# Performance work log

Hardware: AMD Instinct MI355X
Metric: run time of the kernel (lower is better)

## Reference

```python
import jax, jax.numpy as jnp
import numpy as np

B, IN, OUT, K = 512, 65536, 16384, 32

def setup_inputs() -> dict:
    key = jax.random.key(0)
    k1, k2, k3 = jax.random.split(key, 3)
    x = jax.random.normal(k1, (B, IN), dtype=jnp.float32)
    indices = jax.random.randint(k2, (OUT, K), 0, IN, dtype=jnp.int32)
    weight = jax.random.normal(k3, (OUT, K), dtype=jnp.float32) * 0.1
    bias = jnp.zeros((OUT,), dtype=jnp.float32)
    return {"x": x, "indices": indices, "weight": weight, "bias": bias}

def reference(x, indices, weight, bias):
    # Gather per-output feature subsets: (B, OUT, K)
    x_sel = x[:, indices]
    # Weighted sum over K connections per output, plus bias: (B, OUT)
    out = jnp.einsum('bok,ok->bo', x_sel, weight) + bias
    return out
```

## Files before the change

kernel.cpp:

```cpp
#include <hip/hip_runtime.h>

#define B_DIM   512
#define IN_DIM  65536
#define OUT_DIM 16384
#define K_DIM   32

static __device__ __forceinline__ unsigned short f2bf(float f) {
    unsigned u = __builtin_bit_cast(unsigned, f);
    unsigned r = (u + 0x7FFFu + ((u >> 16) & 1u)) >> 16;
    return (unsigned short)r;
}
static __device__ __forceinline__ float bf2f(unsigned short s) {
    return __builtin_bit_cast(float, ((unsigned)s) << 16);
}

#define TB 128
#define TC 64
#define TS 65

__global__ __launch_bounds__(256) void transpose_bf16_k(const float* __restrict__ x,
                                                        unsigned short* __restrict__ xT) {
    __shared__ float tile[TB][TS];
    const int c0 = blockIdx.x * TC;
    const int b0 = blockIdx.y * TB;
    const int t  = threadIdx.x;

    const int col4 = (t & 15) * 4;
    const int br   = t >> 4;
    #pragma unroll
    for (int rr = 0; rr < TB; rr += 16) {
        float4 v = *(const float4*)(x + (size_t)(b0 + br + rr) * IN_DIM + c0 + col4);
        tile[br + rr][col4 + 0] = v.x;
        tile[br + rr][col4 + 1] = v.y;
        tile[br + rr][col4 + 2] = v.z;
        tile[br + rr][col4 + 3] = v.w;
    }
    __syncthreads();

    const int b4 = (t & 31) * 4;
    const int cw = t >> 5;
    #pragma unroll
    for (int cc = 0; cc < TC; cc += 8) {
        const int c = cc + cw;
        ushort4 p;
        p.x = f2bf(tile[b4 + 0][c]);
        p.y = f2bf(tile[b4 + 1][c]);
        p.z = f2bf(tile[b4 + 2][c]);
        p.w = f2bf(tile[b4 + 3][c]);
        *(ushort4*)(xT + (size_t)(c0 + c) * B_DIM + b0 + b4) = p;
    }
}

#define O_TILE 8
#define SE 520

__global__ __launch_bounds__(128) void sparse_main(const unsigned short* __restrict__ xT,
                                                   const int*   __restrict__ idxp,
                                                   const float* __restrict__ wp,
                                                   const float* __restrict__ biasp,
                                                   float*       __restrict__ out) {
    __shared__ float lds[O_TILE][SE];
    const int o_base = blockIdx.x * O_TILE;
    const int t  = threadIdx.x;
    const int b4 = t * 4;

    float4 acc[O_TILE];
    #pragma unroll
    for (int o = 0; o < O_TILE; ++o) acc[o] = make_float4(0.f, 0.f, 0.f, 0.f);

    for (int k = 0; k < K_DIM; ++k) {
        #pragma unroll
        for (int o = 0; o < O_TILE; ++o) {
            const int   idx = idxp[(o_base + o) * K_DIM + k];
            const float w   = wp [(o_base + o) * K_DIM + k];
            const ushort4 v = *(const ushort4*)(xT + (size_t)idx * B_DIM + b4);
            acc[o].x = fmaf(w, bf2f(v.x), acc[o].x);
            acc[o].y = fmaf(w, bf2f(v.y), acc[o].y);
            acc[o].z = fmaf(w, bf2f(v.z), acc[o].z);
            acc[o].w = fmaf(w, bf2f(v.w), acc[o].w);
        }
    }

    #pragma unroll
    for (int o = 0; o < O_TILE; ++o) {
        const float bv = biasp[o_base + o];
        acc[o].x += bv; acc[o].y += bv; acc[o].z += bv; acc[o].w += bv;
        *(float4*)(&lds[o][b4]) = acc[o];
    }
    __syncthreads();

    #pragma unroll
    for (int p = 0; p < 8; ++p) {
        const int q = p * 512 + t * 4;
        const int b = q >> 3;
        const int o = q & 7;
        float4 v;
        v.x = lds[o + 0][b];
        v.y = lds[o + 1][b];
        v.z = lds[o + 2][b];
        v.w = lds[o + 3][b];
        *(float4*)(out + (size_t)b * OUT_DIM + o_base + o) = v;
    }
}

__global__ void sparse_fallback(const float* __restrict__ x,
                                const int*   __restrict__ idxp,
                                const float* __restrict__ wp,
                                const float* __restrict__ biasp,
                                float*       __restrict__ out) {
    const int i = blockIdx.x * blockDim.x + threadIdx.x;
    if (i >= B_DIM * OUT_DIM) return;
    const int b = i / OUT_DIM;
    const int o = i % OUT_DIM;
    float a = biasp[o];
    for (int k = 0; k < K_DIM; ++k) {
        const int idx = idxp[o * K_DIM + k];
        a = fmaf(wp[o * K_DIM + k], x[(size_t)b * IN_DIM + idx], a);
    }
    out[i] = a;
}

extern "C" void kernel_launch(void* const* d_in, const int* in_sizes, int n_in,
                              void* d_out, int out_size, void* d_ws, size_t ws_size,
                              hipStream_t stream) {
    const float* x       = (const float*)d_in[0];
    const int*   indices = (const int*)  d_in[1];
    const float* weight  = (const float*)d_in[2];
    const float* bias    = (const float*)d_in[3];
    float*       out     = (float*)d_out;

    const size_t need = (size_t)IN_DIM * B_DIM * sizeof(unsigned short);
    if (ws_size >= need) {
        unsigned short* xT = (unsigned short*)d_ws;
        dim3 tgrid(IN_DIM / TC, B_DIM / TB);
        transpose_bf16_k<<<tgrid, 256, 0, stream>>>(x, xT);
        sparse_main<<<OUT_DIM / O_TILE, 128, 0, stream>>>(xT, indices, weight, bias, out);
    } else {
        const int n = B_DIM * OUT_DIM;
        sparse_fallback<<<(n + 255) / 256, 256, 0, stream>>>(x, indices, weight, bias, out);
    }
}
```

Baseline: 349.3 us.

## Drop LDS from bf16 transpose and broadcast indices/weights via readlane

The transpose kernel stops staging through shared memory. Each thread now loads 16 consecutive floats of one batch row and writes 16 scalar bf16 values, strided across the transposed layout, with neighbouring lanes writing neighbouring elements. The sparse kernel loads all indices and weights for its 8 outputs with one vector load per lane and broadcasts each value through readlane, instead of issuing per-iteration scalar global loads. It also reorders the loops to o-outer/k-inner and adds an occupancy hint to launch bounds. The risks are that the uncoalesced 2-byte stores and 64B-stride reads in the transpose may be slower than the tiled LDS version, and that the fully unrolled 256-iteration loop raises instruction count and register pressure.

```diff
diff --git a/kernel.cpp b/kernel.cpp
--- a/kernel.cpp
+++ b/kernel.cpp
@@ -10,80 +10,72 @@
     unsigned r = (u + 0x7FFFu + ((u >> 16) & 1u)) >> 16;
     return (unsigned short)r;
 }
-static __device__ __forceinline__ float bf2f(unsigned short s) {
-    return __builtin_bit_cast(float, ((unsigned)s) << 16);
+
+static __device__ __forceinline__ float fcomp(float4 v, int c) {
+    switch (c & 3) { case 0: return v.x; case 1: return v.y; case 2: return v.z; default: return v.w; }
 }
-
-#define TB 128
-#define TC 64
-#define TS 65
 
 __global__ __launch_bounds__(256) void transpose_bf16_k(const float* __restrict__ x,
                                                         unsigned short* __restrict__ xT) {
-    __shared__ float tile[TB][TS];
-    const int c0 = blockIdx.x * TC;
-    const int b0 = blockIdx.y * TB;
+    const int c0 = blockIdx.x * 16;
     const int t  = threadIdx.x;
-
-    const int col4 = (t & 15) * 4;
-    const int br   = t >> 4;
     #pragma unroll
-    for (int rr = 0; rr < TB; rr += 16) {
-        float4 v = *(const float4*)(x + (size_t)(b0 + br + rr) * IN_DIM + c0 + col4);
-        tile[br + rr][col4 + 0] = v.x;
-        tile[br + rr][col4 + 1] = v.y;
-        tile[br + rr][col4 + 2] = v.z;
-        tile[br + rr][col4 + 3] = v.w;
-    }
-    __syncthreads();
-
-    const int b4 = (t & 31) * 4;
-    const int cw = t >> 5;
-    #pragma unroll
-    for (int cc = 0; cc < TC; cc += 8) {
-        const int c = cc + cw;
-        ushort4 p;
-        p.x = f2bf(tile[b4 + 0][c]);
-        p.y = f2bf(tile[b4 + 1][c]);
-        p.z = f2bf(tile[b4 + 2][c]);
-        p.w = f2bf(tile[b4 + 3][c]);
-        *(ushort4*)(xT + (size_t)(c0 + c) * B_DIM + b0 + b4) = p;
+    for (int h = 0; h < 2; ++h) {
+        const int b = h * 256 + t;
+        const float4* p = (const float4*)(x + (size_t)b * IN_DIM + c0);
+        float4 v0 = p[0], v1 = p[1], v2 = p[2], v3 = p[3];
+        #pragma unroll
+        for (int c = 0; c < 16; ++c) {
+            const float4 vv = (c < 4) ? v0 : (c < 8) ? v1 : (c < 12) ? v2 : v3;
+            xT[(size_t)(c0 + c) * B_DIM + b] = f2bf(fcomp(vv, c));
+        }
     }
 }
 
-#define O_TILE 8
 #define SE 520
 
-__global__ __launch_bounds__(128) void sparse_main(const unsigned short* __restrict__ xT,
-                                                   const int*   __restrict__ idxp,
-                                                   const float* __restrict__ wp,
-                                                   const float* __restrict__ biasp,
-                                                   float*       __restrict__ out) {
-    __shared__ float lds[O_TILE][SE];
-    const int o_base = blockIdx.x * O_TILE;
-    const int t  = threadIdx.x;
-    const int b4 = t * 4;
+static __device__ __forceinline__ int icomp(int4 v, int c) {
+    switch (c & 3) { case 0: return v.x; case 1: return v.y; case 2: return v.z; default: return v.w; }
+}
 
-    float4 acc[O_TILE];
+__global__ __launch_bounds__(128, 4) void sparse_main(const unsigned short* __restrict__ xT,
+                                                      const int*   __restrict__ idxp,
+                                                      const float* __restrict__ wp,
+                                                      const float* __restrict__ biasp,
+                                                      float*       __restrict__ out) {
+    __shared__ float lds[8][SE];
+    const int o_blk = blockIdx.x * 8;
+    const int t    = threadIdx.x;
+    const int lane = t & 63;
+    const int b4   = t * 4;
+
+    const int4   iv = ((const int4*)  (idxp + o_blk * K_DIM))[lane];
+    const float4 wv = ((const float4*)(wp   + o_blk * K_DIM))[lane];
+
+    float4 acc[8];
     #pragma unroll
-    for (int o = 0; o < O_TILE; ++o) acc[o] = make_float4(0.f, 0.f, 0.f, 0.f);
+    for (int o = 0; o < 8; ++o) acc[o] = make_float4(0.f, 0.f, 0.f, 0.f);
 
-    for (int k = 0; k < K_DIM; ++k) {
+    #pragma unroll
+    for (int o = 0; o < 8; ++o) {
         #pragma unroll
-        for (int o = 0; o < O_TILE; ++o) {
-            const int   idx = idxp[(o_base + o) * K_DIM + k];
-            const float w   = wp [(o_base + o) * K_DIM + k];
-            const ushort4 v = *(const ushort4*)(xT + (size_t)idx * B_DIM + b4);
-            acc[o].x = fmaf(w, bf2f(v.x), acc[o].x);
-            acc[o].y = fmaf(w, bf2f(v.y), acc[o].y);
-            acc[o].z = fmaf(w, bf2f(v.z), acc[o].z);
-            acc[o].w = fmaf(w, bf2f(v.w), acc[o].w);
+        for (int k = 0; k < K_DIM; ++k) {
+            const int flat = o * K_DIM + k;
+            const int sl   = flat >> 2;
+            const int   sidx = __builtin_amdgcn_readlane(icomp(iv, flat), sl);
+            const float sw   = __int_as_float(
+                __builtin_amdgcn_readlane(__float_as_int(fcomp(wv, flat)), sl));
+            const uint2 u = *(const uint2*)(xT + ((size_t)sidx << 9) + b4);
+            acc[o].x = fmaf(sw, __int_as_float(u.x << 16),          acc[o].x);
+            acc[o].y = fmaf(sw, __int_as_float(u.x & 0xFFFF0000u),  acc[o].y);
+            acc[o].z = fmaf(sw, __int_as_float(u.y << 16),          acc[o].z);
+            acc[o].w = fmaf(sw, __int_as_float(u.y & 0xFFFF0000u),  acc[o].w);
         }
     }
 
     #pragma unroll
-    for (int o = 0; o < O_TILE; ++o) {
-        const float bv = biasp[o_base + o];
+    for (int o = 0; o < 8; ++o) {
+        const float bv = biasp[o_blk + o];
         acc[o].x += bv; acc[o].y += bv; acc[o].z += bv; acc[o].w += bv;
         *(float4*)(&lds[o][b4]) = acc[o];
     }
@@ -99,7 +91,7 @@
         v.y = lds[o + 1][b];
         v.z = lds[o + 2][b];
         v.w = lds[o + 3][b];
-        *(float4*)(out + (size_t)b * OUT_DIM + o_base + o) = v;
+        *(float4*)(out + (size_t)b * OUT_DIM + o_blk + o) = v;
     }
 }
 
@@ -132,9 +124,8 @@
     const size_t need = (size_t)IN_DIM * B_DIM * sizeof(unsigned short);
     if (ws_size >= need) {
         unsigned short* xT = (unsigned short*)d_ws;
-        dim3 tgrid(IN_DIM / TC, B_DIM / TB);
-        transpose_bf16_k<<<tgrid, 256, 0, stream>>>(x, xT);
-        sparse_main<<<OUT_DIM / O_TILE, 128, 0, stream>>>(xT, indices, weight, bias, out);
+        transpose_bf16_k<<<IN_DIM / 16, 256, 0, stream>>>(x, xT);
+        sparse_main<<<OUT_DIM / 8, 128, 0, stream>>>(xT, indices, weight, bias, out);
     } else {
         const int n = B_DIM * OUT_DIM;
         sparse_fallback<<<(n + 255) / 256, 256, 0, stream>>>(x, indices, weight, bias, out);
```

After: 325.5 us. 1.07x faster.
